# Kernel optimization log

Measured on AMD Instinct MI355X. Metric: run time of the kernel, lower is better.

The kernel has to match this reference:

```python
import jax, jax.numpy as jnp
import numpy as np

N = 8192
IN_DIM = 256
OUT_DIM = 64
ALPHA = 0.2  # LeakyReLU negative slope


def setup_inputs() -> dict:
    key = jax.random.key(0)
    k1, k2, k3 = jax.random.split(key, 3)
    h = jax.random.normal(k1, (N, IN_DIM), dtype=jnp.float32)
    adj = jnp.zeros((N, N), dtype=jnp.bool_)  # accepted by forward but unused (faithful to source)
    # xavier_uniform-ish scale for params
    W = jax.random.normal(k2, (IN_DIM, OUT_DIM), dtype=jnp.float32) * (1.414 * (2.0 / (IN_DIM + OUT_DIM)) ** 0.5)
    a = jax.random.normal(k3, (2 * OUT_DIM, 1), dtype=jnp.float32) * (1.414 * (2.0 / (2 * OUT_DIM + 1)) ** 0.5)
    return {"h": h, "adj": adj, "W": W, "a": a}


def reference(h, adj, W, a):
    # Wh: [N, D]
    Wh = h @ W
    d = Wh.shape[1]
    Wh1 = Wh @ a[:d]   # [N, 1]
    Wh2 = Wh @ a[d:]   # [N, 1]
    # e: [N, N] dense additive attention scores (adj is NOT used in the source)
    e = jax.nn.leaky_relu(Wh1 + Wh2.T, negative_slope=ALPHA)
    attention = jax.nn.softmax(e, axis=1)
    # dropout(p=0.6) is identity in eval mode
    h_prime = attention @ Wh  # [N, D]
    return jax.nn.elu(h_prime)
```

## Files before the change

### kernel.cpp

```cpp
#include <hip/hip_runtime.h>
#include <math.h>

#define NN 8192
#define KDIM 256
#define DD 64
#define NB 4096
#define NBLK 256
#define NTHR 512
#define RPB 32
#define CH 32
#define NCH 256
#define LRALPHA 0.2f

__device__ __forceinline__ unsigned f2k(float f) {
    unsigned u = __float_as_uint(f);
    return u ^ ((u >> 31) ? 0xFFFFFFFFu : 0x80000000u);
}
__device__ __forceinline__ float k2f(unsigned k) {
    return __uint_as_float((k & 0x80000000u) ? (k ^ 0x80000000u) : ~k);
}
__device__ __forceinline__ unsigned bucket_of(unsigned key, unsigned kmin, float scale) {
    unsigned d = key - kmin;
    unsigned b = (unsigned)((float)d * scale);
    return b > (NB - 1) ? (NB - 1) : b;
}

__device__ __forceinline__ void  cstf(float* p, float v) { __hip_atomic_store(p, v, __ATOMIC_RELAXED, __HIP_MEMORY_SCOPE_AGENT); }
__device__ __forceinline__ float cldf(const float* p)    { return __hip_atomic_load((float*)p, __ATOMIC_RELAXED, __HIP_MEMORY_SCOPE_AGENT); }

__device__ __forceinline__ void gridbar(unsigned* flags, unsigned* rel, unsigned phase) {
    asm volatile("s_waitcnt vmcnt(0)" ::: "memory");
    __syncthreads();
    const int t = threadIdx.x;
    if (blockIdx.x == 0) {
        if (t == 0)
            __hip_atomic_store(&flags[0], phase, __ATOMIC_RELAXED, __HIP_MEMORY_SCOPE_AGENT);
        if (t < NBLK) {
            while (__hip_atomic_load(&flags[t], __ATOMIC_RELAXED, __HIP_MEMORY_SCOPE_AGENT) < phase)
                __builtin_amdgcn_s_sleep(4);
        }
        __syncthreads();
        if (t == 0)
            __hip_atomic_store(rel, phase, __ATOMIC_RELAXED, __HIP_MEMORY_SCOPE_AGENT);
    } else {
        if (t == 0) {
            __hip_atomic_store(&flags[blockIdx.x], phase, __ATOMIC_RELAXED, __HIP_MEMORY_SCOPE_AGENT);
            while (__hip_atomic_load(rel, __ATOMIC_RELAXED, __HIP_MEMORY_SCOPE_AGENT) < phase)
                __builtin_amdgcn_s_sleep(4);
        }
        __syncthreads();
    }
}

__global__ __launch_bounds__(NTHR, 2) void k_fused(
    const float* __restrict__ h, const float* __restrict__ W,
    const float* __restrict__ a, float* __restrict__ out,
    float* Wh2g, float* sv, float* wnv, float* wpv, float* sg,
    float* cs_neg, float* cs_pos, float* cs_sn, float* cs_sp,
    float* PN, float* SP, float* PNs, float* SPs,
    int* cnt, unsigned* flags, unsigned* rel)
{
    __shared__ int      ls_bstart[NB + 1];
    __shared__ float    ls_wh1[RPB];
    __shared__ float    ls_wh2[RPB];
    __shared__ unsigned ls_ra[8], ls_rb[8];
    __shared__ int      ls_wsum[8];
    __shared__ float    ls_cs[8][2 * DD];
    __shared__ float    ls_css[16];
    __shared__ float    ls_M2, ls_scale;
    __shared__ unsigned ls_kmin;

    const int t = threadIdx.x, bid = blockIdx.x;
    const int wv = t >> 6, lane = t & 63;
    const int rowBase = bid * RPB;

    float myrow[4];
    {
        const int r0 = rowBase + wv * 4;
        float acc0 = 0.f, acc1 = 0.f, acc2 = 0.f, acc3 = 0.f;
        #pragma unroll 2
        for (int k4 = 0; k4 < KDIM / 4; ++k4) {
            float w0 = W[(4 * k4 + 0) * DD + lane];
            float w1 = W[(4 * k4 + 1) * DD + lane];
            float w2 = W[(4 * k4 + 2) * DD + lane];
            float w3 = W[(4 * k4 + 3) * DD + lane];
            float4 h0 = *(const float4*)(h + (size_t)(r0 + 0) * KDIM + 4 * k4);
            float4 h1 = *(const float4*)(h + (size_t)(r0 + 1) * KDIM + 4 * k4);
            float4 h2 = *(const float4*)(h + (size_t)(r0 + 2) * KDIM + 4 * k4);
            float4 h3 = *(const float4*)(h + (size_t)(r0 + 3) * KDIM + 4 * k4);
            acc0 = fmaf(h0.x, w0, acc0); acc0 = fmaf(h0.y, w1, acc0);
            acc0 = fmaf(h0.z, w2, acc0); acc0 = fmaf(h0.w, w3, acc0);
            acc1 = fmaf(h1.x, w0, acc1); acc1 = fmaf(h1.y, w1, acc1);
            acc1 = fmaf(h1.z, w2, acc1); acc1 = fmaf(h1.w, w3, acc1);
            acc2 = fmaf(h2.x, w0, acc2); acc2 = fmaf(h2.y, w1, acc2);
            acc2 = fmaf(h2.z, w2, acc2); acc2 = fmaf(h2.w, w3, acc2);
            acc3 = fmaf(h3.x, w0, acc3); acc3 = fmaf(h3.y, w1, acc3);
            acc3 = fmaf(h3.z, w2, acc3); acc3 = fmaf(h3.w, w3, acc3);
        }
        myrow[0] = acc0; myrow[1] = acc1; myrow[2] = acc2; myrow[3] = acc3;
        float a1 = a[lane], a2 = a[DD + lane];
        #pragma unroll
        for (int i = 0; i < 4; ++i) {
            float r1 = myrow[i] * a1, r2 = myrow[i] * a2;
            #pragma unroll
            for (int off = 32; off > 0; off >>= 1) {
                r1 += __shfl_xor(r1, off, 64);
                r2 += __shfl_xor(r2, off, 64);
            }
            if (lane == 0) {
                cstf(&Wh2g[r0 + i], r2);
                ls_wh1[wv * 4 + i] = r1;
                ls_wh2[wv * 4 + i] = r2;
            }
        }
    }
    gridbar(flags, rel, 1);

    for (int i = t; i < NB; i += NTHR) ls_bstart[i] = 0;
    float v16[16];
    #pragma unroll
    for (int q = 0; q < 16; ++q)
        v16[q] = cldf(&Wh2g[t + q * NTHR]);
    {
        unsigned lmin = 0xFFFFFFFFu, lmax = 0u;
        #pragma unroll
        for (int q = 0; q < 16; ++q) {
            unsigned k = f2k(v16[q]);
            lmin = min(lmin, k); lmax = max(lmax, k);
        }
        #pragma unroll
        for (int off = 32; off > 0; off >>= 1) {
            lmin = min(lmin, (unsigned)__shfl_xor((int)lmin, off, 64));
            lmax = max(lmax, (unsigned)__shfl_xor((int)lmax, off, 64));
        }
        if (lane == 0) { ls_ra[wv] = lmin; ls_rb[wv] = lmax; }
    }
    __syncthreads();
    if (t == 0) {
        unsigned mn = ls_ra[0], mx = ls_rb[0];
        for (int i = 1; i < 8; ++i) { mn = min(mn, ls_ra[i]); mx = max(mx, ls_rb[i]); }
        ls_kmin = mn;
        ls_scale = (float)NB / ((float)(mx - mn) + 1.0f);
        ls_M2 = k2f(mx);
    }
    __syncthreads();
    const unsigned kmin = ls_kmin;
    const float scale = ls_scale;
    const float M2 = ls_M2;

    #pragma unroll
    for (int q = 0; q < 16; ++q)
        atomicAdd(&ls_bstart[bucket_of(f2k(v16[q]), kmin, scale)], 1);
    __syncthreads();
    {
        int s[8]; int tot = 0;
        #pragma unroll
        for (int j = 0; j < 8; ++j) { s[j] = ls_bstart[8 * t + j]; tot += s[j]; }
        int x = tot;
        #pragma unroll
        for (int off = 1; off < 64; off <<= 1) {
            int y = __shfl_up(x, off, 64);
            if (lane >= off) x += y;
        }
        if (lane == 63) ls_wsum[wv] = x;
        __syncthreads();
        int woff = 0;
        for (int w2 = 0; w2 < wv; ++w2) woff += ls_wsum[w2];
        int acc = woff + x - tot;
        #pragma unroll
        for (int j = 0; j < 8; ++j) { ls_bstart[8 * t + j] = acc; acc += s[j]; }
        if (t == 0) ls_bstart[NB] = NN;
    }
    __syncthreads();
    {
        int pos4[4];
        if (lane == 0) {
            #pragma unroll
            for (int i = 0; i < 4; ++i) {
                unsigned b = bucket_of(f2k(ls_wh2[wv * 4 + i]), kmin, scale);
                pos4[i] = ls_bstart[b] + atomicAdd(&cnt[b], 1);
            }
        }
        #pragma unroll
        for (int i = 0; i < 4; ++i) {
            int lr = wv * 4 + i;
            float x = ls_wh2[lr];
            int pos = __shfl(pos4[i], 0, 64);
            cstf(&sg[(size_t)pos * DD + lane], myrow[i]);
            if (lane == 0) {
                cstf(&sv[pos], x);
                cstf(&wnv[pos], expf(LRALPHA * (x - M2)));
                cstf(&wpv[pos], expf(x - M2));
            }
        }
    }
    gridbar(flags, rel, 2);

    {
        int base = bid * CH + wv * 4;
        float g4[4], wn4[4], wp4[4];
        #pragma unroll
        for (int kk = 0; kk < 4; ++kk) {
            int k = base + kk;
            g4[kk]  = cldf(&sg[(size_t)k * DD + lane]);
            wn4[kk] = cldf(&wnv[k]);
            wp4[kk] = cldf(&wpv[k]);
        }
        float an = 0.f, ap = 0.f, sn = 0.f, sp = 0.f;
        #pragma unroll
        for (int kk = 0; kk < 4; ++kk) {
            an = fmaf(wn4[kk], g4[kk], an); ap = fmaf(wp4[kk], g4[kk], ap);
            sn += wn4[kk]; sp += wp4[kk];
        }
        ls_cs[wv][lane] = an; ls_cs[wv][DD + lane] = ap;
        if (lane == 0) { ls_css[wv] = sn; ls_css[8 + wv] = sp; }
        __syncthreads();
        if (wv == 0) {
            float s = 0.f;
            #pragma unroll
            for (int w2 = 0; w2 < 8; ++w2) s += ls_cs[w2][lane];
            cstf(&cs_neg[bid * DD + lane], s);
            if (lane == 0) { float ss = 0.f; for (int w2 = 0; w2 < 8; ++w2) ss += ls_css[w2]; cstf(&cs_sn[bid], ss); }
        } else if (wv == 1) {
            float s = 0.f;
            #pragma unroll
            for (int w2 = 0; w2 < 8; ++w2) s += ls_cs[w2][DD + lane];
            cstf(&cs_pos[bid * DD + lane], s);
            if (lane == 0) { float ss = 0.f; for (int w2 = 0; w2 < 8; ++w2) ss += ls_css[8 + w2]; cstf(&cs_sp[bid], ss); }
        }
    }
    gridbar(flags, rel, 3);

    if (bid == 0) {
        const int c0 = wv * 32;
        float v[32];
        #pragma unroll
        for (int j = 0; j < 32; ++j) v[j] = cldf(&cs_neg[(c0 + j) * DD + lane]);
        float tot = 0.f;
        #pragma unroll
        for (int j = 0; j < 32; ++j) tot += v[j];
        ls_cs[wv][lane] = tot;
        __syncthreads();
        float acc = 0.f;
        for (int w2 = 0; w2 < wv; ++w2) acc += ls_cs[w2][lane];
        #pragma unroll
        for (int j = 0; j < 32; ++j) { cstf(&PN[(c0 + j) * DD + lane], acc); acc += v[j]; }
        if (wv == 7) cstf(&PN[NCH * DD + lane], acc);
    } else if (bid == 1) {
        const int c0 = wv * 32;
        float v[32];
        #pragma unroll
        for (int j = 0; j < 32; ++j) v[j] = cldf(&cs_pos[(c0 + j) * DD + lane]);
        float tot = 0.f;
        #pragma unroll
        for (int j = 0; j < 32; ++j) tot += v[j];
        ls_cs[wv][lane] = tot;
        __syncthreads();
        float acc = 0.f;
        for (int w2 = wv + 1; w2 < 8; ++w2) acc += ls_cs[w2][lane];
        #pragma unroll
        for (int j = 31; j >= 0; --j) { acc += v[j]; cstf(&SP[(c0 + j) * DD + lane], acc); }
        if (wv == 7) cstf(&SP[NCH * DD + lane], 0.f);
    } else if (bid == 2) {
        if (wv == 0) {
            float s[4];
            #pragma unroll
            for (int j = 0; j < 4; ++j) s[j] = cldf(&cs_sn[4 * lane + j]);
            float tot = s[0] + s[1] + s[2] + s[3];
            float x = tot;
            #pragma unroll
            for (int off = 1; off < 64; off <<= 1) {
                float y = __shfl_up(x, off, 64);
                if (lane >= off) x += y;
            }
            float acc = x - tot;
            #pragma unroll
            for (int j = 0; j < 4; ++j) { cstf(&PNs[4 * lane + j], acc); acc += s[j]; }
            if (lane == 63) cstf(&PNs[NCH], acc);
        } else if (wv == 1) {
            float s[4];
            #pragma unroll
            for (int j = 0; j < 4; ++j) s[j] = cldf(&cs_sp[4 * lane + j]);
            float tot = s[0] + s[1] + s[2] + s[3];
            float x = tot;
            #pragma unroll
            for (int off = 1; off < 64; off <<= 1) {
                float y = __shfl_down(x, off, 64);
                if (lane < 64 - off) x += y;
            }
            float acc = x - tot;
            #pragma unroll
            for (int j = 3; j >= 0; --j) { acc += s[j]; cstf(&SPs[4 * lane + j], acc); }
            if (lane == 63) cstf(&SPs[NCH], 0.f);
        }
    }
    gridbar(flags, rel, 4);

    for (int i = 0; i < 4; ++i) {
        int lr = wv * 4 + i;
        int row = rowBase + lr;
        float w1 = ls_wh1[lr];
        float z = w1 + M2;
        float m = (z >= 0.f) ? z : LRALPHA * z;
        float c1 = expf(z - m);
        float c2 = expf(LRALPHA * z - m);
        float tt = -w1;
        unsigned kt = f2k(tt);
        int p0 = 0, p1 = 0;
        if (kt >= kmin) {
            unsigned b = bucket_of(kt, kmin, scale);
            p0 = ls_bstart[b]; p1 = ls_bstart[b + 1];
        }
        int c0f = p0 >> 5;
        int c1e = (p1 + 31) >> 5;
        float nn_ = cldf(&PN[c0f * DD + lane]), dn_ = cldf(&PNs[c0f]);
        float np_ = cldf(&SP[c1e * DD + lane]), dp_ = cldf(&SPs[c1e]);
        for (int base2 = c0f * CH; base2 < c1e * CH; base2 += 8) {
            float sv8[8], wn8[8], wp8[8], g8[8];
            #pragma unroll
            for (int jj = 0; jj < 8; ++jj) {
                int k = base2 + jj;
                sv8[jj] = cldf(&sv[k]);
                wn8[jj] = cldf(&wnv[k]);
                wp8[jj] = cldf(&wpv[k]);
                g8[jj]  = cldf(&sg[(size_t)k * DD + lane]);
            }
            #pragma unroll
            for (int jj = 0; jj < 8; ++jj) {
                if (sv8[jj] <= tt) { nn_ = fmaf(wn8[jj], g8[jj], nn_); dn_ += wn8[jj]; }
                else               { np_ = fmaf(wp8[jj], g8[jj], np_); dp_ += wp8[jj]; }
            }
        }
        float num = c2 * nn_ + c1 * np_;
        float den = c2 * dn_ + c1 * dp_;
        float r = num / den;
        out[(size_t)row * DD + lane] = (r > 0.f) ? r : expm1f(r);
    }
}

extern "C" void kernel_launch(void* const* d_in, const int* in_sizes, int n_in,
                              void* d_out, int out_size, void* d_ws, size_t ws_size,
                              hipStream_t stream)
{
    const float* h = (const float*)d_in[0];
    const float* W = (const float*)d_in[2];
    const float* a = (const float*)d_in[3];
    float* out = (float*)d_out;
    float* ws = (float*)d_ws;

    float* Wh2g   = ws;
    float* sv     = Wh2g + NN;
    float* wnv    = sv + NN;
    float* wpv    = wnv + NN;
    float* sg     = wpv + NN;
    float* cs_neg = sg + (size_t)NN * DD;
    float* cs_pos = cs_neg + NCH * DD;
    float* cs_sn  = cs_pos + NCH * DD;
    float* cs_sp  = cs_sn + NCH;
    float* PN     = cs_sp + NCH;
    float* SP     = PN + (NCH + 1) * DD;
    float* PNs    = SP + (NCH + 1) * DD;
    float* SPs    = PNs + 320;
    unsigned* flags = (unsigned*)(SPs + 320);
    unsigned* rel   = flags + NBLK;
    int*   cnt    = (int*)(rel + 256);

    hipMemsetAsync(flags, 0, (NBLK + 256 + NB) * sizeof(unsigned), stream);
    k_fused<<<NBLK, NTHR, 0, stream>>>(h, W, a, out,
        Wh2g, sv, wnv, wpv, sg,
        cs_neg, cs_pos, cs_sn, cs_sp,
        PN, SP, PNs, SPs,
        cnt, flags, rel);
}
```

Measured before the change: 96.39 us.

## Replace chunk-sum phase with atomics and overlap boundary scan before last barrier

Per-chunk weighted sums are now accumulated with float atomic adds during the scatter, which removes a whole grid-barrier phase and its reload of sorted data. The per-row boundary-chunk scan is moved ahead of the final barrier so it overlaps the prefix-scan phase, and the prefix values are only added afterwards. The sort value and its two weights are packed into one float4 record, and atomic-scope loads are replaced by plain vectorized loads. This saves one grid barrier and some memory traffic. In exchange it adds contended atomics on chunk accumulators, makes float summation order nondeterministic, and relies on plain loads seeing other blocks' writes across the barrier.

Result: slower. 179.0 us (+85.7%).

```diff
diff --git a/kernel.cpp b/kernel.cpp
--- a/kernel.cpp
+++ b/kernel.cpp
@@ -25,8 +25,8 @@
     return b > (NB - 1) ? (NB - 1) : b;
 }
 
-__device__ __forceinline__ void  cstf(float* p, float v) { __hip_atomic_store(p, v, __ATOMIC_RELAXED, __HIP_MEMORY_SCOPE_AGENT); }
-__device__ __forceinline__ float cldf(const float* p)    { return __hip_atomic_load((float*)p, __ATOMIC_RELAXED, __HIP_MEMORY_SCOPE_AGENT); }
+__device__ __forceinline__ void cstf(float* p, float v) { __hip_atomic_store(p, v, __ATOMIC_RELAXED, __HIP_MEMORY_SCOPE_AGENT); }
+__device__ __forceinline__ void afadd(float* p, float v) { __hip_atomic_fetch_add(p, v, __ATOMIC_RELAXED, __HIP_MEMORY_SCOPE_AGENT); }
 
 __device__ __forceinline__ void gridbar(unsigned* flags, unsigned* rel, unsigned phase) {
     asm volatile("s_waitcnt vmcnt(0)" ::: "memory");
@@ -55,7 +55,7 @@
 __global__ __launch_bounds__(NTHR, 2) void k_fused(
     const float* __restrict__ h, const float* __restrict__ W,
     const float* __restrict__ a, float* __restrict__ out,
-    float* Wh2g, float* sv, float* wnv, float* wpv, float* sg,
+    float* Wh2g, float* svp, float* sg,
     float* cs_neg, float* cs_pos, float* cs_sn, float* cs_sp,
     float* PN, float* SP, float* PNs, float* SPs,
     int* cnt, unsigned* flags, unsigned* rel)
@@ -66,7 +66,6 @@
     __shared__ unsigned ls_ra[8], ls_rb[8];
     __shared__ int      ls_wsum[8];
     __shared__ float    ls_cs[8][2 * DD];
-    __shared__ float    ls_css[16];
     __shared__ float    ls_M2, ls_scale;
     __shared__ unsigned ls_kmin;
 
@@ -113,15 +112,22 @@
                 ls_wh2[wv * 4 + i] = r2;
             }
         }
+        if (wv == 0) cstf(&cs_neg[bid * DD + lane], 0.f);
+        else if (wv == 1) cstf(&cs_pos[bid * DD + lane], 0.f);
+        if (t == 0) { cstf(&cs_sn[bid], 0.f); cstf(&cs_sp[bid], 0.f); }
     }
     gridbar(flags, rel, 1);
 
     for (int i = t; i < NB; i += NTHR) ls_bstart[i] = 0;
     float v16[16];
-    #pragma unroll
-    for (int q = 0; q < 16; ++q)
-        v16[q] = cldf(&Wh2g[t + q * NTHR]);
     {
+        const float4* w4p = (const float4*)Wh2g;
+        #pragma unroll
+        for (int q = 0; q < 4; ++q) {
+            float4 x4 = w4p[t * 4 + q];
+            v16[4 * q + 0] = x4.x; v16[4 * q + 1] = x4.y;
+            v16[4 * q + 2] = x4.z; v16[4 * q + 3] = x4.w;
+        }
         unsigned lmin = 0xFFFFFFFFu, lmax = 0u;
         #pragma unroll
         for (int q = 0; q < 16; ++q) {
@@ -185,57 +191,30 @@
         for (int i = 0; i < 4; ++i) {
             int lr = wv * 4 + i;
             float x = ls_wh2[lr];
+            float wn = expf(LRALPHA * (x - M2));
+            float wp = expf(x - M2);
             int pos = __shfl(pos4[i], 0, 64);
-            cstf(&sg[(size_t)pos * DD + lane], myrow[i]);
+            int chunk = pos >> 5;
+            float g = myrow[i];
+            cstf(&sg[(size_t)pos * DD + lane], g);
+            afadd(&cs_neg[chunk * DD + lane], wn * g);
+            afadd(&cs_pos[chunk * DD + lane], wp * g);
             if (lane == 0) {
-                cstf(&sv[pos], x);
-                cstf(&wnv[pos], expf(LRALPHA * (x - M2)));
-                cstf(&wpv[pos], expf(x - M2));
+                cstf(&svp[4 * pos + 0], x);
+                cstf(&svp[4 * pos + 1], wn);
+                cstf(&svp[4 * pos + 2], wp);
+                afadd(&cs_sn[chunk], wn);
+                afadd(&cs_sp[chunk], wp);
             }
         }
     }
     gridbar(flags, rel, 2);
-
-    {
-        int base = bid * CH + wv * 4;
-        float g4[4], wn4[4], wp4[4];
-        #pragma unroll
-        for (int kk = 0; kk < 4; ++kk) {
-            int k = base + kk;
-            g4[kk]  = cldf(&sg[(size_t)k * DD + lane]);
-            wn4[kk] = cldf(&wnv[k]);
-            wp4[kk] = cldf(&wpv[k]);
-        }
-        float an = 0.f, ap = 0.f, sn = 0.f, sp = 0.f;
-        #pragma unroll
-        for (int kk = 0; kk < 4; ++kk) {
-            an = fmaf(wn4[kk], g4[kk], an); ap = fmaf(wp4[kk], g4[kk], ap);
-            sn += wn4[kk]; sp += wp4[kk];
-        }
-        ls_cs[wv][lane] = an; ls_cs[wv][DD + lane] = ap;
-        if (lane == 0) { ls_css[wv] = sn; ls_css[8 + wv] = sp; }
-        __syncthreads();
-        if (wv == 0) {
-            float s = 0.f;
-            #pragma unroll
-            for (int w2 = 0; w2 < 8; ++w2) s += ls_cs[w2][lane];
-            cstf(&cs_neg[bid * DD + lane], s);
-            if (lane == 0) { float ss = 0.f; for (int w2 = 0; w2 < 8; ++w2) ss += ls_css[w2]; cstf(&cs_sn[bid], ss); }
-        } else if (wv == 1) {
-            float s = 0.f;
-            #pragma unroll
-            for (int w2 = 0; w2 < 8; ++w2) s += ls_cs[w2][DD + lane];
-            cstf(&cs_pos[bid * DD + lane], s);
-            if (lane == 0) { float ss = 0.f; for (int w2 = 0; w2 < 8; ++w2) ss += ls_css[8 + w2]; cstf(&cs_sp[bid], ss); }
-        }
-    }
-    gridbar(flags, rel, 3);
 
     if (bid == 0) {
         const int c0 = wv * 32;
         float v[32];
         #pragma unroll
-        for (int j = 0; j < 32; ++j) v[j] = cldf(&cs_neg[(c0 + j) * DD + lane]);
+        for (int j = 0; j < 32; ++j) v[j] = cs_neg[(c0 + j) * DD + lane];
         float tot = 0.f;
         #pragma unroll
         for (int j = 0; j < 32; ++j) tot += v[j];
@@ -250,7 +229,7 @@
         const int c0 = wv * 32;
         float v[32];
         #pragma unroll
-        for (int j = 0; j < 32; ++j) v[j] = cldf(&cs_pos[(c0 + j) * DD + lane]);
+        for (int j = 0; j < 32; ++j) v[j] = cs_pos[(c0 + j) * DD + lane];
         float tot = 0.f;
         #pragma unroll
         for (int j = 0; j < 32; ++j) tot += v[j];
@@ -265,7 +244,7 @@
         if (wv == 0) {
             float s[4];
             #pragma unroll
-            for (int j = 0; j < 4; ++j) s[j] = cldf(&cs_sn[4 * lane + j]);
+            for (int j = 0; j < 4; ++j) s[j] = cs_sn[4 * lane + j];
             float tot = s[0] + s[1] + s[2] + s[3];
             float x = tot;
             #pragma unroll
@@ -280,7 +259,7 @@
         } else if (wv == 1) {
             float s[4];
             #pragma unroll
-            for (int j = 0; j < 4; ++j) s[j] = cldf(&cs_sp[4 * lane + j]);
+            for (int j = 0; j < 4; ++j) s[j] = cs_sp[4 * lane + j];
             float tot = s[0] + s[1] + s[2] + s[3];
             float x = tot;
             #pragma unroll
@@ -294,8 +273,33 @@
             if (lane == 63) cstf(&SPs[NCH], 0.f);
         }
     }
-    gridbar(flags, rel, 4);
-
+    float cn4[4], dn4[4], cp4[4], dp4[4];
+    int c0f4[4], c1e4[4];
+    #pragma unroll
+    for (int i = 0; i < 4; ++i) {
+        int lr = wv * 4 + i;
+        float tt = -ls_wh1[lr];
+        unsigned kt = f2k(tt);
+        int p0 = 0, p1 = 0;
+        if (kt >= kmin) {
+            unsigned b = bucket_of(kt, kmin, scale);
+            p0 = ls_bstart[b]; p1 = ls_bstart[b + 1];
+        }
+        int c0f = p0 >> 5, c1e = (p1 + 31) >> 5;
+        c0f4[i] = c0f; c1e4[i] = c1e;
+        float cn = 0.f, dn = 0.f, cp = 0.f, dp = 0.f;
+        #pragma unroll 8
+        for (int k = c0f * CH; k < c1e * CH; ++k) {
+            float4 q = ((const float4*)svp)[k];
+            float g = sg[(size_t)k * DD + lane];
+            if (q.x <= tt) { cn = fmaf(q.y, g, cn); dn += q.y; }
+            else           { cp = fmaf(q.z, g, cp); dp += q.z; }
+        }
+        cn4[i] = cn; dn4[i] = dn; cp4[i] = cp; dp4[i] = dp;
+    }
+    gridbar(flags, rel, 3);
+
+    #pragma unroll
     for (int i = 0; i < 4; ++i) {
         int lr = wv * 4 + i;
         int row = rowBase + lr;
@@ -304,35 +308,12 @@
         float m = (z >= 0.f) ? z : LRALPHA * z;
         float c1 = expf(z - m);
         float c2 = expf(LRALPHA * z - m);
-        float tt = -w1;
-        unsigned kt = f2k(tt);
-        int p0 = 0, p1 = 0;
-        if (kt >= kmin) {
-            unsigned b = bucket_of(kt, kmin, scale);
-            p0 = ls_bstart[b]; p1 = ls_bstart[b + 1];
-        }
-        int c0f = p0 >> 5;
-        int c1e = (p1 + 31) >> 5;
-        float nn_ = cldf(&PN[c0f * DD + lane]), dn_ = cldf(&PNs[c0f]);
-        float np_ = cldf(&SP[c1e * DD + lane]), dp_ = cldf(&SPs[c1e]);
-        for (int base2 = c0f * CH; base2 < c1e * CH; base2 += 8) {
-            float sv8[8], wn8[8], wp8[8], g8[8];
-            #pragma unroll
-            for (int jj = 0; jj < 8; ++jj) {
-                int k = base2 + jj;
-                sv8[jj] = cldf(&sv[k]);
-                wn8[jj] = cldf(&wnv[k]);
-                wp8[jj] = cldf(&wpv[k]);
-                g8[jj]  = cldf(&sg[(size_t)k * DD + lane]);
-            }
-            #pragma unroll
-            for (int jj = 0; jj < 8; ++jj) {
-                if (sv8[jj] <= tt) { nn_ = fmaf(wn8[jj], g8[jj], nn_); dn_ += wn8[jj]; }
-                else               { np_ = fmaf(wp8[jj], g8[jj], np_); dp_ += wp8[jj]; }
-            }
-        }
-        float num = c2 * nn_ + c1 * np_;
-        float den = c2 * dn_ + c1 * dp_;
+        float pn  = PN[c0f4[i] * DD + lane];
+        float sp  = SP[c1e4[i] * DD + lane];
+        float pns = PNs[c0f4[i]];
+        float sps = SPs[c1e4[i]];
+        float num = c2 * (pn + cn4[i]) + c1 * (sp + cp4[i]);
+        float den = c2 * (pns + dn4[i]) + c1 * (sps + dp4[i]);
         float r = num / den;
         out[(size_t)row * DD + lane] = (r > 0.f) ? r : expm1f(r);
     }
@@ -349,10 +330,8 @@
     float* ws = (float*)d_ws;
 
     float* Wh2g   = ws;
-    float* sv     = Wh2g + NN;
-    float* wnv    = sv + NN;
-    float* wpv    = wnv + NN;
-    float* sg     = wpv + NN;
+    float* svp    = Wh2g + NN;
+    float* sg     = svp + 4 * NN;
     float* cs_neg = sg + (size_t)NN * DD;
     float* cs_pos = cs_neg + NCH * DD;
     float* cs_sn  = cs_pos + NCH * DD;
@@ -367,7 +346,7 @@
 
     hipMemsetAsync(flags, 0, (NBLK + 256 + NB) * sizeof(unsigned), stream);
     k_fused<<<NBLK, NTHR, 0, stream>>>(h, W, a, out,
-        Wh2g, sv, wnv, wpv, sg,
+        Wh2g, svp, sg,
         cs_neg, cs_pos, cs_sn, cs_sp,
         PN, SP, PNs, SPs,
         cnt, flags, rel);
```
